# Optimization experiments

Hardware: AMD Instinct MI355X
Metric: run time of the kernel (lower is better)

## Reference

```python
import jax, jax.numpy as jnp
import numpy as np

# FrictionConfig constants (chosen in init_kwargs)
K_STEPS = 4
ETA = 0.1
ETA_DECAY = 0.9
MU_MAX = 10.0
SMOOTH_LAMBDA = 0.1
RADIUS = 8
B, S, H = 4, 2048, 1024
INNER = max(H // 2, 32)  # 512


def _build_window_edges(length, radius):
    chunks = []
    for d in range(1, radius + 1):
        i = np.arange(length - d, dtype=np.int32)
        chunks.append(np.stack([i, i + d], axis=1))
    return np.concatenate(chunks, axis=0)  # [E, 2]


def setup_inputs() -> dict:
    key = jax.random.key(0)
    ks = jax.random.split(key, 8)
    hidden = jax.random.normal(ks[0], (B, S, H), dtype=jnp.float32)
    attention_mask = jnp.ones((B, S), dtype=jnp.int32)
    edges = jnp.asarray(_build_window_edges(S, RADIUS))
    # edge_mlp: Linear(2, INNER) -> GELU -> Linear(INNER, 1)
    W1 = jax.random.normal(ks[1], (2, INNER), dtype=jnp.float32) * (1.0 / np.sqrt(2))
    b1 = jnp.zeros((INNER,), dtype=jnp.float32)
    W2 = jax.random.normal(ks[2], (INNER, 1), dtype=jnp.float32) * (1.0 / np.sqrt(INNER))
    b2 = jnp.zeros((1,), dtype=jnp.float32)
    # q_proj: Linear(H, H)
    Wq = jax.random.normal(ks[3], (H, H), dtype=jnp.float32) * (1.0 / np.sqrt(H))
    bq = jnp.zeros((H,), dtype=jnp.float32)
    # LayerNorm
    gamma = jnp.ones((H,), dtype=jnp.float32)
    beta = jnp.zeros((H,), dtype=jnp.float32)
    return {"hidden": hidden, "attention_mask": attention_mask, "edges": edges,
            "Wq": Wq, "bq": bq, "W1": W1, "b1": b1, "W2": W2, "b2": b2,
            "gamma": gamma, "beta": beta}


def _edge_weights(h, ei, ej, W1, b1, W2, b2):
    hi = h[ei]  # [E, H]
    hj = h[ej]
    diff = hi - hj
    dist = jnp.linalg.norm(diff, axis=-1, keepdims=True)           # [E, 1]
    ni = jnp.maximum(jnp.linalg.norm(hi, axis=-1), 1e-6)
    nj = jnp.maximum(jnp.linalg.norm(hj, axis=-1), 1e-6)
    cos = (jnp.sum(hi * hj, axis=-1) / (ni * nj))[:, None]         # [E, 1]
    feats = jnp.concatenate([dist, cos], axis=-1)                  # [E, 2]
    z = jax.nn.gelu(feats @ W1 + b1, approximate=False) @ W2 + b2  # [E, 1]
    return jax.nn.softplus(z) + 1e-5


def _laplacian(h, ei, ej, mu):
    n = h.shape[0]
    weighted = mu * (h[ei] - h[ej])  # [E, H]
    # normalize_laplacian = True
    w = mu[:, 0]
    deg = jnp.zeros((n,), h.dtype).at[ei].add(w).at[ej].add(w)
    inv_sqrt = jnp.maximum(deg, 1e-6) ** -0.5
    weighted = weighted * (inv_sqrt[ei] * inv_sqrt[ej])[:, None]
    lap = jnp.zeros_like(h).at[ei].add(weighted).at[ej].add(-weighted)
    return lap


def _smooth(s):
    left = jnp.concatenate([s[:1], s[:-1]], axis=0)
    right = jnp.concatenate([s[1:], s[-1:]], axis=0)
    return s - SMOOTH_LAMBDA * (2.0 * s - left - right)


def _layernorm(x, gamma, beta):
    m = x.mean(axis=-1, keepdims=True)
    v = x.var(axis=-1, keepdims=True)
    return (x - m) * jax.lax.rsqrt(v + 1e-5) * gamma + beta


def _run_single(h, ei, ej, Wq, bq, W1, b1, W2, b2, gamma, beta):
    q = h @ Wq + bq
    state = h
    mu = None
    for step in range(K_STEPS):
        mu = _edge_weights(state, ei, ej, W1, b1, W2, b2)  # recompute_mu=True
        mu = jnp.minimum(mu, MU_MAX)
        lap = _laplacian(state, ei, ej, mu)
        eta = ETA * (ETA_DECAY ** step)
        state = state - eta * (lap - q)
        state = _smooth(state)
    out = _layernorm(state + h, gamma, beta)
    diffs = state[ei] - state[ej]
    energy = 0.5 * jnp.sum(mu[:, 0] * jnp.sum(diffs * diffs, axis=-1))
    return out, energy


def reference(hidden, attention_mask, edges, Wq, bq, W1, b1, W2, b2, gamma, beta):
    # All masks are full-length, so edges are identical across batch and
    # the outer Python batch loop vectorizes to a vmap.
    ei, ej = edges[:, 0], edges[:, 1]
    outputs, energy = jax.vmap(
        lambda h: _run_single(h, ei, ej, Wq, bq, W1, b1, W2, b2, gamma, beta)
    )(hidden)
    return outputs, energy
```

## Files before the change

### kernel.cpp

```cpp
#include <hip/hip_runtime.h>

#define BB 4
#define SS 2048
#define HH 1024
#define TQ 32
#define TU 32
#define CW 256

typedef unsigned short u16;
typedef __bf16 bf16x8 __attribute__((ext_vector_type(8)));
typedef float f32x4 __attribute__((ext_vector_type(4)));

__device__ __forceinline__ float b2f(u16 u){
  union { unsigned int i; float f; } v; v.i = ((unsigned int)u) << 16; return v.f;
}
__device__ __forceinline__ u16 f2b(float f){
  union { float f; unsigned int i; } v; v.f = f;
  unsigned int x = v.i;
  return (u16)((x + 0x7fffu + ((x >> 16) & 1u)) >> 16);
}
__device__ __forceinline__ float4 u4f(ushort4 v){
  float4 o; o.x = b2f(v.x); o.y = b2f(v.y); o.z = b2f(v.z); o.w = b2f(v.w); return o;
}
__device__ __forceinline__ ushort4 f4u(float4 v){
  ushort4 o; o.x = f2b(v.x); o.y = f2b(v.y); o.z = f2b(v.z); o.w = f2b(v.w); return o;
}
__device__ __forceinline__ float wave_sum(float v){
  #pragma unroll
  for(int m = 32; m > 0; m >>= 1) v += __shfl_xor(v, m);
  return v;
}
__device__ __forceinline__ float pread(const void* p, int i, int f){
  return f ? b2f(((const u16*)p)[i]) : ((const float*)p)[i];
}
__device__ __forceinline__ int dflag(const void* gm){
  return (((const u16*)gm)[0] == 0x3F80u) ? 1 : 0;
}
__device__ __forceinline__ void gload16(const void* g, void* l){
  __builtin_amdgcn_global_load_lds((const __attribute__((address_space(1))) unsigned int*)g,
                                   (__attribute__((address_space(3))) unsigned int*)l, 16, 0, 0);
}

__global__ __launch_bounds__(256) void k_setup(const void* hidden, u16* __restrict__ s,
                                               const void* Wq, u16* __restrict__ Wt,
                                               const void* bq, const void* W1, const void* b1,
                                               const void* W2, const void* b2, const void* gm,
                                               const void* bt,
                                               float* bqc, float* W1c, float* b1c, float* W2c,
                                               float* b2c, float* gmc, float* btc,
                                               float* partials, int* ecnt){
  __shared__ u16 t[32][33];
  int f = dflag(gm);
  int bid = blockIdx.x, tid = threadIdx.x;
  if(bid < 8192){
    size_t i4 = (size_t)bid*256 + tid;
    if(f){
      ((ushort4*)s)[i4] = ((const ushort4*)hidden)[i4];
    } else {
      ((ushort4*)s)[i4] = f4u(((const float4*)hidden)[i4]);
    }
  } else if(bid < 8192 + 1024){
    int bi = bid - 8192;
    int bx = bi & 31, by = bi >> 5;
    int tx = tid & 31, ty = tid >> 5;
    #pragma unroll
    for(int r = 0; r < 32; r += 8){
      int idx = (by*32 + ty + r)*HH + bx*32 + tx;
      float v = f ? b2f(((const u16*)Wq)[idx]) : ((const float*)Wq)[idx];
      t[ty + r][tx] = f2b(v);
    }
    __syncthreads();
    #pragma unroll
    for(int r = 0; r < 32; r += 8)
      Wt[(size_t)(bx*32 + ty + r)*HH + by*32 + tx] = t[tx][ty + r];
  } else {
    for(int i = tid; i < 1024; i += 256) bqc[i] = pread(bq, i, f);
    for(int i = tid; i < 1024; i += 256) W1c[i] = pread(W1, i, f);
    for(int i = tid; i <  512; i += 256) b1c[i] = pread(b1, i, f);
    for(int i = tid; i <  512; i += 256) W2c[i] = pread(W2, i, f);
    if(tid == 0) b2c[0] = pread(b2, 0, f);
    for(int i = tid; i < 1024; i += 256) gmc[i] = pread(gm, i, f);
    for(int i = tid; i < 1024; i += 256) btc[i] = pread(bt, i, f);
    if(tid < BB){ partials[tid] = 0.f; ecnt[tid] = 0; }
  }
}

__global__ __launch_bounds__(256) void k_qgemm(const u16* __restrict__ A, const u16* __restrict__ Wt,
                                               const float* __restrict__ bqc, u16* __restrict__ q){
  __shared__ u16 lA[128*32];
  __shared__ u16 lB[128*32];
  int m0 = blockIdx.x*128, n0 = blockIdx.y*128;
  int tid  = threadIdx.x;
  int wave = tid >> 6, lane = tid & 63;
  int wm = (wave >> 1)*64, wn = (wave & 1)*64;
  int quad = lane >> 4, l16 = lane & 15;
  int srow = tid >> 2;
  int scol = (tid & 3)*8;

  f32x4 acc[4][4];
  #pragma unroll
  for(int i = 0; i < 4; i++)
    #pragma unroll
    for(int j = 0; j < 4; j++) acc[i][j] = (f32x4){0.f,0.f,0.f,0.f};

  for(int k0 = 0; k0 < HH; k0 += 32){
    __syncthreads();
    gload16(A  + (size_t)(m0 + srow     )*HH + k0 + scol, &lA[ srow     *32 + scol]);
    gload16(A  + (size_t)(m0 + srow + 64)*HH + k0 + scol, &lA[(srow+64) *32 + scol]);
    gload16(Wt + (size_t)(n0 + srow     )*HH + k0 + scol, &lB[ srow     *32 + scol]);
    gload16(Wt + (size_t)(n0 + srow + 64)*HH + k0 + scol, &lB[(srow+64) *32 + scol]);
    __syncthreads();
    bf16x8 af[4];
    #pragma unroll
    for(int mt = 0; mt < 4; mt++)
      af[mt] = *(const bf16x8*)&lA[(wm + mt*16 + l16)*32 + quad*8];
    #pragma unroll
    for(int nt = 0; nt < 4; nt++){
      bf16x8 bf = *(const bf16x8*)&lB[(wn + nt*16 + l16)*32 + quad*8];
      #pragma unroll
      for(int mt = 0; mt < 4; mt++)
        acc[mt][nt] = __builtin_amdgcn_mfma_f32_16x16x32_bf16(af[mt], bf, acc[mt][nt], 0, 0, 0);
    }
  }
  #pragma unroll
  for(int nt = 0; nt < 4; nt++){
    int col = n0 + wn + nt*16 + l16;
    float bqv = bqc[col];
    #pragma unroll
    for(int mt = 0; mt < 4; mt++){
      #pragma unroll
      for(int r = 0; r < 4; r++){
        int row = m0 + wm + mt*16 + quad*4 + r;
        q[(size_t)row*HH + col] = f2b(acc[mt][nt][r] + bqv);
      }
    }
  }
}

__global__ __launch_bounds__(512) void k_gram_mu(const u16* __restrict__ s,
                                                 const float* __restrict__ W1c, const float* __restrict__ b1c,
                                                 const float* __restrict__ W2c, const float* __restrict__ b2c,
                                                 float* __restrict__ mu){
  __shared__ float Gband[40*9];
  __shared__ float4 wpk[512];
  int b = blockIdx.z, i0 = blockIdx.x*TQ;
  int tid = threadIdx.x, wave = tid >> 6, lane = tid & 63;

  wpk[tid] = make_float4(W1c[tid]     * 0.70710678118654752f,
                         W1c[512+tid] * 0.70710678118654752f,
                         b1c[tid]     * 0.70710678118654752f,
                         W2c[tid]     * 0.70710678118654752f);

  if(wave < 4){
    int ti = wave >> 1;
    int tj = (wave + 1) >> 1;
    int quad = lane >> 4, l16 = lane & 15;
    int ra = i0 + ti*16 + l16; if(ra > SS-1) ra = SS-1;
    int rb = i0 + tj*16 + l16; if(rb > SS-1) rb = SS-1;
    const u16* ar = s + ((size_t)b*SS + ra)*HH + quad*8;
    const u16* br = s + ((size_t)b*SS + rb)*HH + quad*8;
    f32x4 acc = (f32x4){0.f,0.f,0.f,0.f};
    #pragma unroll 8
    for(int k0 = 0; k0 < HH; k0 += 32){
      bf16x8 af = *(const bf16x8*)(ar + k0);
      bf16x8 bf = *(const bf16x8*)(br + k0);
      acc = __builtin_amdgcn_mfma_f32_16x16x32_bf16(af, bf, acc, 0, 0, 0);
    }
    #pragma unroll
    for(int r = 0; r < 4; r++){
      int gr = ti*16 + quad*4 + r;
      int dd = tj*16 + l16 - gr;
      if(dd >= 0 && dd <= 8) Gband[gr*9 + dd] = acc[r];
    }
  } else {
    for(int rr = wave - 4; rr < 8; rr += 4){
      int r = 32 + rr;
      int row = i0 + r; if(row > SS-1) row = SS-1;
      const ushort4* rp = (const ushort4*)(s + ((size_t)b*SS + row)*HH);
      float a = 0.f;
      #pragma unroll
      for(int c = 0; c < 4; c++){
        float4 v = u4f(rp[lane + 64*c]);
        a += v.x*v.x + v.y*v.y + v.z*v.z + v.w*v.w;
      }
      a = wave_sum(a);
      if(lane == 0) Gband[r*9] = a;
    }
  }
  __syncthreads();

  int el = tid >> 2, qd = tid & 3;
  int dl = el >> 5, k = el & 31;
  int d = blockIdx.y*4 + dl + 1;
  bool valid = (i0 + k + d) < SS;
  float gii = Gband[k*9], gjj = Gband[(k+d)*9], gij = Gband[k*9 + d];
  float dist = sqrtf(fmaxf(gii + gjj - 2.f*gij, 0.f));
  float ni = fmaxf(sqrtf(gii), 1e-6f);
  float nj = fmaxf(sqrtf(gjj), 1e-6f);
  float cosv = gij * __builtin_amdgcn_rcpf(ni * nj);
  float acc = 0.f;
  const float4* wp = &wpk[qd*128];
  #pragma unroll 4
  for(int j0 = 0; j0 < 128; j0++){
    float4 wv = wp[j0];
    float x  = fmaf(dist, wv.x, fmaf(cosv, wv.y, wv.z));
    float ax = fabsf(x);
    float t  = __builtin_amdgcn_rcpf(fmaf(0.3275911f, ax, 1.f));
    float poly = ((((1.061405429f*t - 1.453152027f)*t + 1.421413741f)*t
                   - 0.284496736f)*t + 0.254829592f)*t;
    float ape = ax * poly * __expf(-ax*ax);
    acc = fmaf(x + ax - ape, wv.w, acc);
  }
  acc += __shfl_xor(acc, 1);
  acc += __shfl_xor(acc, 2);
  if(qd == 0 && valid){
    float z  = acc + b2c[0];
    float sp = fmaxf(z, 0.f) + __logf(1.f + __expf(-fabsf(z)));
    mu[((size_t)b*8 + (d-1))*SS + (i0 + k)] = fminf(sp + 1e-5f, 10.0f);
  }
}

__global__ __launch_bounds__(256, 4) void k_upsm(const u16* __restrict__ sIn, u16* __restrict__ sOut,
                                                 const u16* __restrict__ q, const float* __restrict__ mu,
                                                 float eta){
  __shared__ u16 st[50*CW];
  __shared__ float invsS[50];
  __shared__ float muS[58*8];
  int i0 = blockIdx.x*TU, c0 = blockIdx.y*CW, b = blockIdx.z;
  int tid = threadIdx.x;

  for(int idx = tid; idx < 58*8; idx += 256){
    int ir = idx >> 3, d = (idx & 7) + 1;
    int i = i0 - 17 + ir;
    float v = 0.f;
    if(i >= 0 && i + d < SS) v = mu[((size_t)b*8 + d-1)*SS + i];
    muS[idx] = v;
  }
  for(int idx = tid; idx < 50*(CW/4); idx += 256){
    int r = idx / (CW/4), cc = idx % (CW/4);
    int i = i0 - 9 + r;
    ushort4 v = {0,0,0,0};
    if(i >= 0 && i < SS) v = *(const ushort4*)(sIn + ((size_t)b*SS + i)*HH + c0 + cc*4);
    ((ushort4*)st)[idx] = v;
  }
  __syncthreads();
  if(tid < 50){
    int ir = tid + 8;
    float deg = 0.f;
    #pragma unroll
    for(int d = 1; d <= 8; d++){
      deg += muS[ir*8 + d-1];
      deg += muS[(ir-d)*8 + d-1];
    }
    invsS[tid] = 1.0f / sqrtf(fmaxf(deg, 1e-6f));
  }
  __syncthreads();

  int rq = tid >> 6, lane = tid & 63;
  float4 ua = {0,0,0,0}, ub = {0,0,0,0}, uc = {0,0,0,0};
  #pragma unroll
  for(int k = 0; k < 10; k++){
    int ur = rq*8 + k;
    int i  = i0 - 1 + ur;
    float4 o = {0.f,0.f,0.f,0.f};
    if(i >= 0 && i < SS){
      int sr = ur + 8, vr = ur + 8, mr = ur + 16;
      float inv_i = invsS[vr];
      float4 si = u4f(((const ushort4*)(st + (size_t)sr*CW))[lane]);
      float A = 0.f;
      float4 acc = {0.f,0.f,0.f,0.f};
      #pragma unroll
      for(int d = 1; d <= 8; d++){
        float cR = muS[mr*8 + d-1]     * inv_i        * invsS[vr+d];
        float cL = muS[(mr-d)*8 + d-1] * invsS[vr-d]  * inv_i;
        A += cR + cL;
        float4 vR = u4f(((const ushort4*)(st + (size_t)(sr+d)*CW))[lane]);
        float4 vL = u4f(((const ushort4*)(st + (size_t)(sr-d)*CW))[lane]);
        acc.x -= cR*vR.x + cL*vL.x; acc.y -= cR*vR.y + cL*vL.y;
        acc.z -= cR*vR.z + cL*vL.z; acc.w -= cR*vR.w + cL*vL.w;
      }
      acc.x += A*si.x; acc.y += A*si.y; acc.z += A*si.z; acc.w += A*si.w;
      float4 qv = u4f(*(const ushort4*)(q + ((size_t)b*SS + i)*HH + c0 + lane*4));
      o.x = si.x - eta*(acc.x - qv.x);
      o.y = si.y - eta*(acc.y - qv.y);
      o.z = si.z - eta*(acc.z - qv.z);
      o.w = si.w - eta*(acc.w - qv.w);
    }
    ua = ub; ub = uc; uc = o;
    if(k >= 2){
      int rr = rq*8 + k - 2;
      int iout = i0 + rr;
      float4 cc2 = ub;
      float4 l  = (iout > 0)     ? ua : cc2;
      float4 r4 = (iout < SS-1)  ? uc : cc2;
      float4 oo;
      oo.x = cc2.x - 0.1f*(2.f*cc2.x - l.x - r4.x);
      oo.y = cc2.y - 0.1f*(2.f*cc2.y - l.y - r4.y);
      oo.z = cc2.z - 0.1f*(2.f*cc2.z - l.z - r4.z);
      oo.w = cc2.w - 0.1f*(2.f*cc2.w - l.w - r4.w);
      *(ushort4*)(sOut + ((size_t)b*SS + iout)*HH + c0 + lane*4) = f4u(oo);
    }
  }
}

__global__ __launch_bounds__(256) void k_out(const u16* __restrict__ sA, const void* __restrict__ hraw,
                                             const float* __restrict__ gmc, const float* __restrict__ btc,
                                             void* __restrict__ outp, const void* __restrict__ gmraw){
  int f = dflag(gmraw);
  int b = blockIdx.x >> 11, i = blockIdx.x & (SS-1);
  int tid = threadIdx.x;
  size_t row = (size_t)b*SS + i;
  float4 sv = u4f(((const ushort4*)(sA + row*HH))[tid]);
  float4 hv;
  if(f) hv = u4f(((const ushort4*)((const u16*)hraw + row*HH))[tid]);
  else  hv = ((const float4*)((const float*)hraw + row*HH))[tid];
  float x0 = sv.x + hv.x, x1 = sv.y + hv.y, x2 = sv.z + hv.z, x3 = sv.w + hv.w;

  __shared__ float sh[4];
  int wv = tid >> 6, lane = tid & 63;
  float lsum = wave_sum(x0 + x1 + x2 + x3);
  if(lane == 0) sh[wv] = lsum;
  __syncthreads();
  float mean = (sh[0] + sh[1] + sh[2] + sh[3]) * (1.f/HH);
  __syncthreads();
  float d0 = x0-mean, d1 = x1-mean, d2 = x2-mean, d3 = x3-mean;
  float lsq = wave_sum(d0*d0 + d1*d1 + d2*d2 + d3*d3);
  if(lane == 0) sh[wv] = lsq;
  __syncthreads();
  float var = (sh[0] + sh[1] + sh[2] + sh[3]) * (1.f/HH);
  float sc = 1.0f / sqrtf(var + 1e-5f);

  int col = tid*4;
  float4 o;
  o.x = d0*sc*gmc[col+0] + btc[col+0];
  o.y = d1*sc*gmc[col+1] + btc[col+1];
  o.z = d2*sc*gmc[col+2] + btc[col+2];
  o.w = d3*sc*gmc[col+3] + btc[col+3];
  if(f) ((ushort4*)((u16*)outp + row*HH))[tid] = f4u(o);
  else  ((float4*)((float*)outp + row*HH))[tid] = o;
}

__global__ __launch_bounds__(512) void k_energy(const u16* __restrict__ s, const float* __restrict__ mu,
                                                float* __restrict__ partials, int* __restrict__ ecnt,
                                                const void* __restrict__ gmraw, void* __restrict__ outp){
  __shared__ float Gband[40*9];
  __shared__ float wacc[8];
  int b = blockIdx.y, i0 = blockIdx.x*TQ;
  int tid = threadIdx.x, wave = tid >> 6, lane = tid & 63;

  if(wave < 4){
    int ti = wave >> 1;
    int tj = (wave + 1) >> 1;
    int quad = lane >> 4, l16 = lane & 15;
    int ra = i0 + ti*16 + l16; if(ra > SS-1) ra = SS-1;
    int rb = i0 + tj*16 + l16; if(rb > SS-1) rb = SS-1;
    const u16* ar = s + ((size_t)b*SS + ra)*HH + quad*8;
    const u16* br = s + ((size_t)b*SS + rb)*HH + quad*8;
    f32x4 acc = (f32x4){0.f,0.f,0.f,0.f};
    #pragma unroll 8
    for(int k0 = 0; k0 < HH; k0 += 32){
      bf16x8 af = *(const bf16x8*)(ar + k0);
      bf16x8 bf = *(const bf16x8*)(br + k0);
      acc = __builtin_amdgcn_mfma_f32_16x16x32_bf16(af, bf, acc, 0, 0, 0);
    }
    #pragma unroll
    for(int r = 0; r < 4; r++){
      int gr = ti*16 + quad*4 + r;
      int dd = tj*16 + l16 - gr;
      if(dd >= 0 && dd <= 8) Gband[gr*9 + dd] = acc[r];
    }
  } else {
    for(int rr = wave - 4; rr < 8; rr += 4){
      int r = 32 + rr;
      int row = i0 + r; if(row > SS-1) row = SS-1;
      const ushort4* rp = (const ushort4*)(s + ((size_t)b*SS + row)*HH);
      float a = 0.f;
      #pragma unroll
      for(int c = 0; c < 4; c++){
        float4 v = u4f(rp[lane + 64*c]);
        a += v.x*v.x + v.y*v.y + v.z*v.z + v.w*v.w;
      }
      a = wave_sum(a);
      if(lane == 0) Gband[r*9] = a;
    }
  }
  __syncthreads();

  int d = wave + 1;
  int k = lane;
  float esum = 0.f;
  if(k < 32 && (i0 + k + d) < SS){
    float d2 = fmaxf(Gband[k*9] + Gband[(k+d)*9] - 2.f*Gband[k*9 + d], 0.f);
    esum = mu[((size_t)b*8 + (d-1))*SS + (i0 + k)] * d2;
  }
  esum = wave_sum(esum);
  if(lane == 0) wacc[wave] = esum;
  __syncthreads();
  if(tid == 0){
    float t = 0.f;
    #pragma unroll
    for(int w2 = 0; w2 < 8; w2++) t += wacc[w2];
    atomicAdd(&partials[b], t);
    __threadfence();
    int old = atomicAdd(&ecnt[b], 1);
    if(old == (SS/TQ) - 1){
      float tot = atomicAdd(&partials[b], 0.0f);
      float e = 0.5f * tot;
      int f = dflag(gmraw);
      if(f) ((u16*)outp)[(size_t)BB*SS*HH + b] = f2b(e);
      else  ((float*)outp)[(size_t)BB*SS*HH + b] = e;
    }
  }
}

extern "C" void kernel_launch(void* const* d_in, const int* in_sizes, int n_in,
                              void* d_out, int out_size, void* d_ws, size_t ws_size,
                              hipStream_t stream) {
  const void* hidden = d_in[0];
  const void* Wq  = d_in[3];
  const void* bq  = d_in[4];
  const void* W1  = d_in[5];
  const void* b1  = d_in[6];
  const void* W2  = d_in[7];
  const void* b2v = d_in[8];
  const void* gamma = d_in[9];
  const void* beta  = d_in[10];

  char* w = (char*)d_ws;
  u16*   q   = (u16*)w;   w += (size_t)BB*SS*HH*2;
  u16*   sA  = (u16*)w;   w += (size_t)BB*SS*HH*2;
  u16*   Wt  = (u16*)w;   w += (size_t)HH*HH*2;
  float* mu  = (float*)w; w += (size_t)BB*8*SS*4;
  float* partials = (float*)w; w += BB*4;
  int*   ecnt = (int*)w;  w += BB*4;
  float* bqc = (float*)w; w += 1024*4;
  float* W1c = (float*)w; w += 1024*4;
  float* b1c = (float*)w; w += 512*4;
  float* W2c = (float*)w; w += 512*4;
  float* b2c = (float*)w; w += 4;
  float* gmc = (float*)w; w += 1024*4;
  float* btc = (float*)w; w += 1024*4;
  u16* sB = (u16*)d_out;

  k_setup<<<8192 + 1024 + 1, 256, 0, stream>>>(hidden, sA, Wq, Wt, bq, W1, b1, W2, b2v,
                                               gamma, beta, bqc, W1c, b1c, W2c, b2c, gmc, btc,
                                               partials, ecnt);
  k_qgemm<<<dim3(BB*SS/128, HH/128), 256, 0, stream>>>(sA, Wt, bqc, q);

  const float etas[4] = {0.1f, 0.09f, 0.081f, 0.0729f};
  for(int step = 0; step < 4; step++){
    const u16* cur = (step & 1) ? sB : sA;
    u16*       nxt = (step & 1) ? sA : sB;
    k_gram_mu<<<dim3(SS/TQ, 2, BB), 512, 0, stream>>>(cur, W1c, b1c, W2c, b2c, mu);
    k_upsm   <<<dim3(SS/TU, HH/CW, BB), 256, 0, stream>>>(cur, nxt, q, mu, etas[step]);
  }
  k_out   <<<BB*SS, 256, 0, stream>>>(sA, hidden, gmc, btc, d_out, gamma);
  k_energy<<<dim3(SS/TQ, BB), 512, 0, stream>>>(sA, mu, partials, ecnt, gamma, d_out);
}
```

Baseline: 402.1 us.

## Sort MLP hidden units by sign-stability key to skip erf on saturated units

Precomputes per-hidden-unit keys in setup and sorts the edge MLP weights so that units whose preactivation is guaranteed large for the wave's minimum distance use a cheap ReLU-style path instead of the erf polynomial. k_mu now handles all 8 diagonals per block with 2 threads per edge, instead of launching two blocks that each recomputed the Gram band. Also widens the state loads in k_upsm to 16 bytes and uses a single global counter for energy finalization. The saturation bound drops the erf tail, so results carry a small approximation error. It also assumes cos lies in [-1,1] and that the distance bound holds.

```diff
diff --git a/kernel.cpp b/kernel.cpp
--- a/kernel.cpp
+++ b/kernel.cpp
@@ -40,16 +40,26 @@
   __builtin_amdgcn_global_load_lds((const __attribute__((address_space(1))) unsigned int*)g,
                                    (__attribute__((address_space(3))) unsigned int*)l, 16, 0, 0);
 }
+__device__ __forceinline__ float  g_load(const float* p){
+  return __hip_atomic_load(p, __ATOMIC_RELAXED, __HIP_MEMORY_SCOPE_AGENT);
+}
+__device__ __forceinline__ float  part_add(float* p, float v){
+  return __hip_atomic_fetch_add(p, v, __ATOMIC_RELAXED, __HIP_MEMORY_SCOPE_AGENT);
+}
+__device__ __forceinline__ int    cnt_add(int* p){
+  return __hip_atomic_fetch_add(p, 1, __ATOMIC_RELAXED, __HIP_MEMORY_SCOPE_AGENT);
+}
 
 __global__ __launch_bounds__(256) void k_setup(const void* hidden, u16* __restrict__ s,
                                                const void* Wq, u16* __restrict__ Wt,
                                                const void* bq, const void* W1, const void* b1,
                                                const void* W2, const void* b2, const void* gm,
                                                const void* bt,
-                                               float* bqc, float* W1c, float* b1c, float* W2c,
-                                               float* b2c, float* gmc, float* btc,
+                                               float* bqc, float* b2c, float* gmc, float* btc,
+                                               float4* mlp4s, float* mkeys,
                                                float* partials, int* ecnt){
   __shared__ u16 t[32][33];
+  __shared__ float ka[512], kb[512], kc[512], kw[512], kk[512];
   int f = dflag(gm);
   int bid = blockIdx.x, tid = threadIdx.x;
   if(bid < 8192){
@@ -75,13 +85,30 @@
       Wt[(size_t)(bx*32 + ty + r)*HH + by*32 + tx] = t[tx][ty + r];
   } else {
     for(int i = tid; i < 1024; i += 256) bqc[i] = pread(bq, i, f);
-    for(int i = tid; i < 1024; i += 256) W1c[i] = pread(W1, i, f);
-    for(int i = tid; i <  512; i += 256) b1c[i] = pread(b1, i, f);
-    for(int i = tid; i <  512; i += 256) W2c[i] = pread(W2, i, f);
     if(tid == 0) b2c[0] = pread(b2, 0, f);
     for(int i = tid; i < 1024; i += 256) gmc[i] = pread(gm, i, f);
     for(int i = tid; i < 1024; i += 256) btc[i] = pread(bt, i, f);
-    if(tid < BB){ partials[tid] = 0.f; ecnt[tid] = 0; }
+    if(tid < BB) partials[tid] = 0.f;
+    if(tid == 0) ecnt[0] = 0;
+    const float is2 = 0.70710678118654752f;
+    for(int j = tid; j < 512; j += 256){
+      float a = pread(W1, j, f)       * is2;
+      float b = pread(W1, 512 + j, f) * is2;
+      float c = pread(b1, j, f)       * is2;
+      float w = pread(W2, j, f)       * is2;
+      ka[j] = a; kb[j] = b; kc[j] = c; kw[j] = w;
+      float aa = fabsf(a);
+      kk[j] = (aa > 0.f) ? (4.f + fabsf(b) + fabsf(c)) * __builtin_amdgcn_rcpf(aa) : 3e38f;
+    }
+    __syncthreads();
+    for(int j = tid; j < 512; j += 256){
+      float kj = kk[j];
+      int r = 0;
+      for(int k = 0; k < 512; k++)
+        r += (kk[k] < kj) || (kk[k] == kj && k < j);
+      mlp4s[r] = make_float4(ka[j], kb[j], kc[j], kw[j]);
+      mkeys[r] = kj;
+    }
   }
 }
 
@@ -137,20 +164,9 @@
   }
 }
 
-__global__ __launch_bounds__(512) void k_gram_mu(const u16* __restrict__ s,
-                                                 const float* __restrict__ W1c, const float* __restrict__ b1c,
-                                                 const float* __restrict__ W2c, const float* __restrict__ b2c,
-                                                 float* __restrict__ mu){
-  __shared__ float Gband[40*9];
-  __shared__ float4 wpk[512];
-  int b = blockIdx.z, i0 = blockIdx.x*TQ;
-  int tid = threadIdx.x, wave = tid >> 6, lane = tid & 63;
-
-  wpk[tid] = make_float4(W1c[tid]     * 0.70710678118654752f,
-                         W1c[512+tid] * 0.70710678118654752f,
-                         b1c[tid]     * 0.70710678118654752f,
-                         W2c[tid]     * 0.70710678118654752f);
-
+__device__ __forceinline__ void gram_band8(const u16* __restrict__ s, int b, int i0,
+                                           float* __restrict__ Gband, int tid){
+  int wave = tid >> 6, lane = tid & 63;
   if(wave < 4){
     int ti = wave >> 1;
     int tj = (wave + 1) >> 1;
@@ -187,33 +203,61 @@
       if(lane == 0) Gband[r*9] = a;
     }
   }
-  __syncthreads();
-
-  int el = tid >> 2, qd = tid & 3;
-  int dl = el >> 5, k = el & 31;
-  int d = blockIdx.y*4 + dl + 1;
+}
+
+__global__ __launch_bounds__(512) void k_mu(const u16* __restrict__ s,
+                                            const float4* __restrict__ mlp4s,
+                                            const float* __restrict__ mkeys,
+                                            const float* __restrict__ b2c,
+                                            float* __restrict__ mu){
+  __shared__ float Gband[40*9];
+  __shared__ float4 wpk[512];
+  __shared__ float skey[512];
+  int b = blockIdx.y, i0 = blockIdx.x*TQ;
+  int tid = threadIdx.x;
+  wpk[tid] = mlp4s[tid]; skey[tid] = mkeys[tid];
+  gram_band8(s, b, i0, Gband, tid);
+  __syncthreads();
+
+  int e = tid >> 1, h = tid & 1;
+  int d = (e >> 5) + 1, k = e & 31;
   bool valid = (i0 + k + d) < SS;
   float gii = Gband[k*9], gjj = Gband[(k+d)*9], gij = Gband[k*9 + d];
   float dist = sqrtf(fmaxf(gii + gjj - 2.f*gij, 0.f));
   float ni = fmaxf(sqrtf(gii), 1e-6f);
   float nj = fmaxf(sqrtf(gjj), 1e-6f);
   float cosv = gij * __builtin_amdgcn_rcpf(ni * nj);
+  if(!valid){ dist = 3e38f; cosv = 0.f; }
+
+  float wmin = dist;
+  #pragma unroll
+  for(int m = 32; m > 0; m >>= 1) wmin = fminf(wmin, __shfl_xor(wmin, m));
+  int lo = 0, hi = 512;
+  while(lo < hi){ int mid = (lo + hi) >> 1; if(skey[mid] <= wmin) lo = mid + 1; else hi = mid; }
+  int cut = lo - h*256; cut = (cut < 0) ? 0 : (cut > 256 ? 256 : cut);
+
+  const float4* wp = &wpk[h*256];
   float acc = 0.f;
-  const float4* wp = &wpk[qd*128];
+  int j = 0;
   #pragma unroll 4
-  for(int j0 = 0; j0 < 128; j0++){
-    float4 wv = wp[j0];
+  for(; j < cut; j++){
+    float4 wv = wp[j];
+    float x = fmaf(dist, wv.x, fmaf(cosv, wv.y, wv.z));
+    acc = fmaf(x + fabsf(x), wv.w, acc);
+  }
+  #pragma unroll 2
+  for(; j < 256; j++){
+    float4 wv = wp[j];
     float x  = fmaf(dist, wv.x, fmaf(cosv, wv.y, wv.z));
     float ax = fabsf(x);
-    float t  = __builtin_amdgcn_rcpf(fmaf(0.3275911f, ax, 1.f));
-    float poly = ((((1.061405429f*t - 1.453152027f)*t + 1.421413741f)*t
-                   - 0.284496736f)*t + 0.254829592f)*t;
+    float tt = __builtin_amdgcn_rcpf(fmaf(0.3275911f, ax, 1.f));
+    float poly = ((((1.061405429f*tt - 1.453152027f)*tt + 1.421413741f)*tt
+                   - 0.284496736f)*tt + 0.254829592f)*tt;
     float ape = ax * poly * __expf(-ax*ax);
     acc = fmaf(x + ax - ape, wv.w, acc);
   }
   acc += __shfl_xor(acc, 1);
-  acc += __shfl_xor(acc, 2);
-  if(qd == 0 && valid){
+  if(h == 0 && valid){
     float z  = acc + b2c[0];
     float sp = fmaxf(z, 0.f) + __logf(1.f + __expf(-fabsf(z)));
     mu[((size_t)b*8 + (d-1))*SS + (i0 + k)] = fminf(sp + 1e-5f, 10.0f);
@@ -229,19 +273,19 @@
   int i0 = blockIdx.x*TU, c0 = blockIdx.y*CW, b = blockIdx.z;
   int tid = threadIdx.x;
 
+  for(int idx = tid; idx < 50*(CW/8); idx += 256){
+    int r = idx >> 5, cc = idx & 31;
+    int i = i0 - 9 + r;
+    uint4 v = {0,0,0,0};
+    if(i >= 0 && i < SS) v = *(const uint4*)(sIn + ((size_t)b*SS + i)*HH + c0 + cc*8);
+    ((uint4*)st)[idx] = v;
+  }
   for(int idx = tid; idx < 58*8; idx += 256){
     int ir = idx >> 3, d = (idx & 7) + 1;
     int i = i0 - 17 + ir;
     float v = 0.f;
     if(i >= 0 && i + d < SS) v = mu[((size_t)b*8 + d-1)*SS + i];
     muS[idx] = v;
-  }
-  for(int idx = tid; idx < 50*(CW/4); idx += 256){
-    int r = idx / (CW/4), cc = idx % (CW/4);
-    int i = i0 - 9 + r;
-    ushort4 v = {0,0,0,0};
-    if(i >= 0 && i < SS) v = *(const ushort4*)(sIn + ((size_t)b*SS + i)*HH + c0 + cc*4);
-    ((ushort4*)st)[idx] = v;
   }
   __syncthreads();
   if(tid < 50){
@@ -342,48 +386,12 @@
 
 __global__ __launch_bounds__(512) void k_energy(const u16* __restrict__ s, const float* __restrict__ mu,
                                                 float* __restrict__ partials, int* __restrict__ ecnt,
-                                                const void* __restrict__ gmraw, void* __restrict__ outp){
+                                                void* __restrict__ outp, const void* __restrict__ gmraw){
   __shared__ float Gband[40*9];
   __shared__ float wacc[8];
   int b = blockIdx.y, i0 = blockIdx.x*TQ;
   int tid = threadIdx.x, wave = tid >> 6, lane = tid & 63;
-
-  if(wave < 4){
-    int ti = wave >> 1;
-    int tj = (wave + 1) >> 1;
-    int quad = lane >> 4, l16 = lane & 15;
-    int ra = i0 + ti*16 + l16; if(ra > SS-1) ra = SS-1;
-    int rb = i0 + tj*16 + l16; if(rb > SS-1) rb = SS-1;
-    const u16* ar = s + ((size_t)b*SS + ra)*HH + quad*8;
-    const u16* br = s + ((size_t)b*SS + rb)*HH + quad*8;
-    f32x4 acc = (f32x4){0.f,0.f,0.f,0.f};
-    #pragma unroll 8
-    for(int k0 = 0; k0 < HH; k0 += 32){
-      bf16x8 af = *(const bf16x8*)(ar + k0);
-      bf16x8 bf = *(const bf16x8*)(br + k0);
-      acc = __builtin_amdgcn_mfma_f32_16x16x32_bf16(af, bf, acc, 0, 0, 0);
-    }
-    #pragma unroll
-    for(int r = 0; r < 4; r++){
-      int gr = ti*16 + quad*4 + r;
-      int dd = tj*16 + l16 - gr;
-      if(dd >= 0 && dd <= 8) Gband[gr*9 + dd] = acc[r];
-    }
-  } else {
-    for(int rr = wave - 4; rr < 8; rr += 4){
-      int r = 32 + rr;
-      int row = i0 + r; if(row > SS-1) row = SS-1;
-      const ushort4* rp = (const ushort4*)(s + ((size_t)b*SS + row)*HH);
-      float a = 0.f;
-      #pragma unroll
-      for(int c = 0; c < 4; c++){
-        float4 v = u4f(rp[lane + 64*c]);
-        a += v.x*v.x + v.y*v.y + v.z*v.z + v.w*v.w;
-      }
-      a = wave_sum(a);
-      if(lane == 0) Gband[r*9] = a;
-    }
-  }
+  gram_band8(s, b, i0, Gband, tid);
   __syncthreads();
 
   int d = wave + 1;
@@ -400,15 +408,19 @@
     float t = 0.f;
     #pragma unroll
     for(int w2 = 0; w2 < 8; w2++) t += wacc[w2];
-    atomicAdd(&partials[b], t);
-    __threadfence();
-    int old = atomicAdd(&ecnt[b], 1);
-    if(old == (SS/TQ) - 1){
-      float tot = atomicAdd(&partials[b], 0.0f);
-      float e = 0.5f * tot;
+    part_add(&partials[b], t);
+  }
+  __syncthreads();
+  if(tid == 0){
+    int old = cnt_add(ecnt);
+    if(old == (SS/TQ)*BB - 1){
       int f = dflag(gmraw);
-      if(f) ((u16*)outp)[(size_t)BB*SS*HH + b] = f2b(e);
-      else  ((float*)outp)[(size_t)BB*SS*HH + b] = e;
+      #pragma unroll
+      for(int bb = 0; bb < BB; bb++){
+        float e = 0.5f * g_load(&partials[bb]);
+        if(f) ((u16*)outp)[(size_t)BB*SS*HH + bb] = f2b(e);
+        else  ((float*)outp)[(size_t)BB*SS*HH + bb] = e;
+      }
     }
   }
 }
@@ -427,33 +439,32 @@
   const void* beta  = d_in[10];
 
   char* w = (char*)d_ws;
-  u16*   q   = (u16*)w;   w += (size_t)BB*SS*HH*2;
-  u16*   sA  = (u16*)w;   w += (size_t)BB*SS*HH*2;
-  u16*   Wt  = (u16*)w;   w += (size_t)HH*HH*2;
-  float* mu  = (float*)w; w += (size_t)BB*8*SS*4;
-  float* partials = (float*)w; w += BB*4;
-  int*   ecnt = (int*)w;  w += BB*4;
-  float* bqc = (float*)w; w += 1024*4;
-  float* W1c = (float*)w; w += 1024*4;
-  float* b1c = (float*)w; w += 512*4;
-  float* W2c = (float*)w; w += 512*4;
-  float* b2c = (float*)w; w += 4;
-  float* gmc = (float*)w; w += 1024*4;
-  float* btc = (float*)w; w += 1024*4;
+  u16*   q   = (u16*)w;     w += (size_t)BB*SS*HH*2;
+  u16*   sA  = (u16*)w;     w += (size_t)BB*SS*HH*2;
+  u16*   Wt  = (u16*)w;     w += (size_t)HH*HH*2;
+  float* mu  = (float*)w;   w += (size_t)BB*8*SS*4;
+  float4* mlp4s = (float4*)w; w += 512*16;
+  float* mkeys = (float*)w; w += 512*4;
+  float* bqc = (float*)w;   w += 1024*4;
+  float* b2c = (float*)w;   w += 16;
+  float* gmc = (float*)w;   w += 1024*4;
+  float* btc = (float*)w;   w += 1024*4;
+  float* partials = (float*)w; w += 16;
+  int*   ecnt = (int*)w;    w += 16;
   u16* sB = (u16*)d_out;
 
   k_setup<<<8192 + 1024 + 1, 256, 0, stream>>>(hidden, sA, Wq, Wt, bq, W1, b1, W2, b2v,
-                                               gamma, beta, bqc, W1c, b1c, W2c, b2c, gmc, btc,
-                                               partials, ecnt);
+                                               gamma, beta, bqc, b2c, gmc, btc,
+                                               mlp4s, mkeys, partials, ecnt);
   k_qgemm<<<dim3(BB*SS/128, HH/128), 256, 0, stream>>>(sA, Wt, bqc, q);
 
   const float etas[4] = {0.1f, 0.09f, 0.081f, 0.0729f};
   for(int step = 0; step < 4; step++){
     const u16* cur = (step & 1) ? sB : sA;
     u16*       nxt = (step & 1) ? sA : sB;
-    k_gram_mu<<<dim3(SS/TQ, 2, BB), 512, 0, stream>>>(cur, W1c, b1c, W2c, b2c, mu);
-    k_upsm   <<<dim3(SS/TU, HH/CW, BB), 256, 0, stream>>>(cur, nxt, q, mu, etas[step]);
+    k_mu  <<<dim3(SS/TQ, BB), 512, 0, stream>>>(cur, mlp4s, mkeys, b2c, mu);
+    k_upsm<<<dim3(SS/TU, HH/CW, BB), 256, 0, stream>>>(cur, nxt, q, mu, etas[step]);
   }
   k_out   <<<BB*SS, 256, 0, stream>>>(sA, hidden, gmc, btc, d_out, gamma);
-  k_energy<<<dim3(SS/TQ, BB), 512, 0, stream>>>(sA, mu, partials, ecnt, gamma, d_out);
-}
+  k_energy<<<dim3(SS/TQ, BB), 512, 0, stream>>>(sA, mu, partials, ecnt, d_out, gamma);
+}
```

Measured after the change: 391.8 us. -2.6%, faster.
